# Kernel optimization log

Hardware: AMD Instinct MI355X
Metric: run time of the kernel (lower is better)

The kernel has to match this reference:

```python
import jax, jax.numpy as jnp
import numpy as np
import math

N_HEADS = 4
GROUPS = 32
EPS = 1e-5


def group_norm(x, w, b, groups=GROUPS):
    B, C, H, W = x.shape
    xg = x.reshape(B, groups, C // groups, H, W)
    mu = xg.mean(axis=(2, 3, 4), keepdims=True)
    var = xg.var(axis=(2, 3, 4), keepdims=True)
    xn = ((xg - mu) / jnp.sqrt(var + EPS)).reshape(B, C, H, W)
    return xn * w[None, :, None, None] + b[None, :, None, None]


def setup_inputs() -> dict:
    key = jax.random.key(0)
    ks = jax.random.split(key, 8)
    B, C, H, W = 4, 256, 64, 64
    s = 1.0 / math.sqrt(C)
    return {
        "x": jax.random.normal(ks[0], (B, C, H, W), jnp.float32),
        "context": jax.random.normal(ks[1], (B, C, H, W), jnp.float32),
        "gn_q_w": jnp.ones((C,), jnp.float32),
        "gn_q_b": jnp.zeros((C,), jnp.float32),
        "gn_ctx_w": jnp.ones((C,), jnp.float32),
        "gn_ctx_b": jnp.zeros((C,), jnp.float32),
        "Wq": jax.random.normal(ks[2], (C, C), jnp.float32) * s,
        "Wk": jax.random.normal(ks[3], (C, C), jnp.float32) * s,
        "Wv": jax.random.normal(ks[4], (C, C), jnp.float32) * s,
        "Wo": jax.random.normal(ks[5], (C, C), jnp.float32) * s,
        "bo": jnp.zeros((C,), jnp.float32),
    }


def reference(x, context, gn_q_w, gn_q_b, gn_ctx_w, gn_ctx_b, Wq, Wk, Wv, Wo, bo):
    B, C, H, W = x.shape
    hd = C // N_HEADS
    # 1x1 convs == channel matmuls
    q = jnp.einsum('oc,bchw->bohw', Wq, group_norm(x, gn_q_w, gn_q_b))
    k = jnp.einsum('oc,bchw->bohw', Wk, group_norm(context, gn_ctx_w, gn_ctx_b))
    v = jnp.einsum('oc,bchw->bohw', Wv, context)
    q = q.reshape(B, N_HEADS, hd, H * W)
    k = k.reshape(B, N_HEADS, hd, H * W)
    v = v.reshape(B, N_HEADS, hd, H * W)
    attn = jnp.einsum('bncd,bnce->bnde', q, k) / math.sqrt(hd)  # [B,n,HW,HW]
    attn = jax.nn.softmax(attn, axis=-1)
    out = jnp.einsum('bnde,bnce->bncd', attn, v).reshape(B, C, H, W)
    out = jnp.einsum('oc,bchw->bohw', Wo, out) + bo[None, :, None, None]
    return x + out
```

## Files before the change

kernel.cpp:

```cpp
#include <hip/hip_runtime.h>

typedef __bf16 bf16x8 __attribute__((ext_vector_type(8)));
typedef __bf16 bf16x2 __attribute__((ext_vector_type(2)));
typedef float f32x2 __attribute__((ext_vector_type(2)));
typedef float f32x4 __attribute__((ext_vector_type(4)));
typedef float f32x16 __attribute__((ext_vector_type(16)));

#define DEV static __device__ __forceinline__

DEV unsigned short f2bf(float f) {
  union { float f; unsigned int u; } v; v.f = f;
  unsigned int u = v.u;
  return (unsigned short)((u + 0x7FFFu + ((u >> 16) & 1u)) >> 16);
}

DEV bf16x8 ldb8(const unsigned short* p) { return *reinterpret_cast<const bf16x8*>(p); }

DEV bf16x8 ldsb8(const unsigned short* base, int byteoff) {
  return *reinterpret_cast<const bf16x8*>((const char*)base + byteoff);
}

DEV f32x4 mfma(bf16x8 a, bf16x8 b, f32x4 c) {
  return __builtin_amdgcn_mfma_f32_16x16x32_bf16(a, b, c, 0, 0, 0);
}
DEV f32x16 mfma32(bf16x8 a, bf16x8 b, f32x16 c) {
  return __builtin_amdgcn_mfma_f32_32x32x16_bf16(a, b, c, 0, 0, 0);
}

DEV float fexp2(float x) {
  float r;
  asm("v_exp_f32 %0, %1" : "=v"(r) : "v"(x));
  return r;
}

DEV unsigned cvtpk(float a, float b) {
  f32x2 t = {a, b};
  bf16x2 r = __builtin_convertvector(t, bf16x2);
  return __builtin_bit_cast(unsigned, r);
}

DEV bf16x8 pack4(unsigned w0, unsigned w1, unsigned w2, unsigned w3) {
  union { unsigned u[4]; bf16x8 v; } x;
  x.u[0] = w0; x.u[1] = w1; x.u[2] = w2; x.u[3] = w3;
  return x.v;
}

DEV f32x16 zero16() {
  f32x16 z;
#pragma unroll
  for (int i = 0; i < 16; ++i) z[i] = 0.f;
  return z;
}

__global__ __launch_bounds__(1024) void gn_stats_kernel(
    const float* __restrict__ x, const float* __restrict__ ctx,
    const float* __restrict__ gqw, const float* __restrict__ gqb,
    const float* __restrict__ gcw, const float* __restrict__ gcb,
    float* __restrict__ ssbuf) {
  int id = blockIdx.x;
  int tensor = id >> 7;
  int bg = id & 127;
  int b = bg >> 5, g = bg & 31;
  const float* src = tensor ? ctx : x;
  const float* gw = tensor ? gcw : gqw;
  const float* gb = tensor ? gcb : gqb;
  float* scale = ssbuf + tensor * 2048;
  float* shift = scale + 1024;

  const float* base = src + (size_t)(b * 256 + g * 8) * 4096;
  int tid = threadIdx.x;
  float s = 0.f, sq = 0.f;
#pragma unroll
  for (int i = 0; i < 8; ++i) {
    float4 v = *reinterpret_cast<const float4*>(base + (i * 1024 + tid) * 4);
    s += v.x + v.y + v.z + v.w;
    sq = __builtin_fmaf(v.x, v.x, sq);
    sq = __builtin_fmaf(v.y, v.y, sq);
    sq = __builtin_fmaf(v.z, v.z, sq);
    sq = __builtin_fmaf(v.w, v.w, sq);
  }
#pragma unroll
  for (int sh = 32; sh; sh >>= 1) {
    s += __shfl_down(s, sh);
    sq += __shfl_down(sq, sh);
  }
  __shared__ float rs[16], rq[16], mr[2];
  int w = tid >> 6;
  if ((tid & 63) == 0) { rs[w] = s; rq[w] = sq; }
  __syncthreads();
  if (tid == 0) {
    float S = 0.f, Q = 0.f;
#pragma unroll
    for (int i = 0; i < 16; ++i) { S += rs[i]; Q += rq[i]; }
    float mean = S * (1.f / 32768.f);
    float var = __builtin_fmaf(-mean, mean, Q * (1.f / 32768.f));
    mr[0] = mean;
    mr[1] = rsqrtf(var + 1e-5f);
  }
  __syncthreads();
  if (tid < 8) {
    int c = g * 8 + tid;
    float sc = gw[c] * mr[1];
    scale[b * 256 + c] = sc;
    shift[b * 256 + c] = __builtin_fmaf(-mr[0], sc, gb[c]);
  }
}

template <int OUTMODE>
__global__ __launch_bounds__(1024) void proj_kernel(
    const float* __restrict__ W, const float* __restrict__ in,
    const float* __restrict__ scale, const float* __restrict__ shift,
    unsigned short* __restrict__ out, float wscale) {
  __shared__ unsigned short Alds[128][72];
  __shared__ unsigned short Blds[128][72];
  const int b = blockIdx.z;
  const int o0 = blockIdx.y * 128;
  const int p0 = blockIdx.x * 128;
  const int tid = threadIdx.x;
  const int w = tid >> 6, lane = tid & 63;
  const int g = lane >> 4, l15 = lane & 15;
  const int oh = (w >> 2) * 32, ph = (w & 3) * 32;

  f32x4 acc[2][2];
#pragma unroll
  for (int i = 0; i < 2; ++i)
#pragma unroll
    for (int j = 0; j < 2; ++j) acc[i][j] = (f32x4){0.f, 0.f, 0.f, 0.f};

  for (int kk = 0; kk < 4; ++kk) {
    const int c0 = kk * 64;
    __syncthreads();
#pragma unroll
    for (int i = 0; i < 2; ++i) {
      int idx = i * 1024 + tid;
      int row = idx >> 4, col4 = (idx & 15) * 4;
      float4 wv = *reinterpret_cast<const float4*>(&W[(size_t)(o0 + row) * 256 + c0 + col4]);
      ushort4 bv = {f2bf(wv.x * wscale), f2bf(wv.y * wscale),
                    f2bf(wv.z * wscale), f2bf(wv.w * wscale)};
      *reinterpret_cast<ushort4*>(&Alds[row][col4]) = bv;
    }
#pragma unroll
    for (int i = 0; i < 2; ++i) {
      int idx = i * 1024 + tid;
      int cc = idx >> 5, p4 = (idx & 31) * 4;
      int c = c0 + cc;
      float4 xv = *reinterpret_cast<const float4*>(&in[((size_t)b * 256 + c) * 4096 + p0 + p4]);
      float sc = 1.f, sh = 0.f;
      if (scale) { sc = scale[b * 256 + c]; sh = shift[b * 256 + c]; }
      Blds[p4 + 0][cc] = f2bf(__builtin_fmaf(xv.x, sc, sh));
      Blds[p4 + 1][cc] = f2bf(__builtin_fmaf(xv.y, sc, sh));
      Blds[p4 + 2][cc] = f2bf(__builtin_fmaf(xv.z, sc, sh));
      Blds[p4 + 3][cc] = f2bf(__builtin_fmaf(xv.w, sc, sh));
    }
    __syncthreads();
#pragma unroll
    for (int kf = 0; kf < 2; ++kf) {
      bf16x8 av[2], bv[2];
#pragma unroll
      for (int mf = 0; mf < 2; ++mf) av[mf] = ldb8(&Alds[oh + mf * 16 + l15][kf * 32 + g * 8]);
#pragma unroll
      for (int nf = 0; nf < 2; ++nf) bv[nf] = ldb8(&Blds[ph + nf * 16 + l15][kf * 32 + g * 8]);
#pragma unroll
      for (int mf = 0; mf < 2; ++mf)
#pragma unroll
        for (int nf = 0; nf < 2; ++nf) acc[mf][nf] = mfma(av[mf], bv[nf], acc[mf][nf]);
    }
  }
#pragma unroll
  for (int mf = 0; mf < 2; ++mf)
#pragma unroll
    for (int nf = 0; nf < 2; ++nf) {
      int o = o0 + oh + mf * 16 + g * 4;
      int p = p0 + ph + nf * 16 + l15;
      if (OUTMODE == 0) {
        int h = o >> 6, ch = o & 63;
        ushort4 vv = {f2bf(acc[mf][nf][0]), f2bf(acc[mf][nf][1]),
                      f2bf(acc[mf][nf][2]), f2bf(acc[mf][nf][3])};
        *reinterpret_cast<ushort4*>(&out[(((size_t)b * 4 + h) * 4096 + p) * 64 + ch]) = vv;
      } else {
#pragma unroll
        for (int r = 0; r < 4; ++r) {
          int oo = o + r;
          out[(((size_t)b * 4 + (oo >> 6)) * 64 + (oo & 63)) * 4096 + p] = f2bf(acc[mf][nf][r]);
        }
      }
    }
}

DEV void stageK32(const unsigned short* kg, int e0, char* ldsbase, int tidg) {
  int o = tidg * 16;
  int r = o >> 7;
  int col = (o & 127) ^ ((r & 7) << 4);
  const char* src = (const char*)(kg + (size_t)(e0 + r) * 64) + col;
  __builtin_amdgcn_global_load_lds(
      (__attribute__((address_space(1))) void*)src,
      (__attribute__((address_space(3))) void*)(ldsbase + (tidg >> 6) * 1024), 16, 0, 0);
}

DEV void stageV32(const unsigned short* vg, int e0, char* ldsbase, int tidg) {
  int o = tidg * 16;
  int c = o >> 6;
  int slotL = ((o >> 4) & 3) ^ ((c >> 1) & 3);
  const char* src = (const char*)(vg + (size_t)c * 4096 + e0 + slotL * 8);
  __builtin_amdgcn_global_load_lds(
      (__attribute__((address_space(1))) void*)src,
      (__attribute__((address_space(3))) void*)(ldsbase + (tidg >> 6) * 1024), 16, 0, 0);
}

__global__ __launch_bounds__(1024) void attn_kernel(
    const unsigned short* __restrict__ QT, const unsigned short* __restrict__ KT,
    const unsigned short* __restrict__ V, unsigned short* __restrict__ OT) {
  __shared__ __align__(16) char smem[67584];
  const int bh = blockIdx.x;
  const int tid = threadIdx.x;
  const int w = tid >> 6, lane = tid & 63;
  const int g = w >> 2, wl = w & 3;
  const int tidg = tid & 255;
  const int hi = lane >> 5, l31 = lane & 31;
  const int d = blockIdx.y * 128 + wl * 32 + l31;

  char* Kb0 = smem + g * 16384;
  char* Kb1 = Kb0 + 4096;
  char* Vb0 = Kb0 + 8192;
  char* Vb1 = Kb0 + 12288;

  const unsigned short* kg = KT + (size_t)bh * 4096 * 64;
  const unsigned short* vg = V + (size_t)bh * 64 * 4096;

  bf16x8 q[4];
#pragma unroll
  for (int ks = 0; ks < 4; ++ks)
    q[ks] = ldb8(&QT[((size_t)bh * 4096 + d) * 64 + ks * 16 + hi * 8]);

  f32x16 oacc[2];
  oacc[0] = zero16();
  oacc[1] = zero16();
  float lsum = 0.f;
  const int kswz = (l31 & 7) << 4;
  const int vswz = ((l31 >> 1) & 3) << 4;
  const int E0 = g * 1024;

  auto compute = [&](const char* kb_, const char* vb_) {
    const unsigned short* kb = (const unsigned short*)kb_;
    const unsigned short* vb = (const unsigned short*)vb_;
    f32x16 st = zero16();
    __builtin_amdgcn_s_setprio(1);
#pragma unroll
    for (int ks = 0; ks < 4; ++ks) {
      bf16x8 k0 = ldsb8(kb, l31 * 128 + ((ks * 32 + hi * 16) ^ kswz));
      st = mfma32(k0, q[ks], st);
    }
    __builtin_amdgcn_s_setprio(0);

#pragma unroll
    for (int i = 0; i < 16; ++i) st[i] = fexp2(st[i]);

    bf16x8 pf[2];
#pragma unroll
    for (int sh = 0; sh < 2; ++sh) {
      const int rb = sh * 8;
      unsigned a0 = cvtpk(st[rb + 0], st[rb + 1]);
      unsigned b0 = cvtpk(st[rb + 4], st[rb + 5]);
      unsigned a1 = cvtpk(st[rb + 2], st[rb + 3]);
      unsigned b1 = cvtpk(st[rb + 6], st[rb + 7]);
      auto r0 = __builtin_amdgcn_permlane32_swap(a0, b0, false, false);
      auto r1 = __builtin_amdgcn_permlane32_swap(a1, b1, false, false);
      pf[sh] = pack4(r0[0], r1[0], r0[1], r1[1]);
    }

    float ss[8];
#pragma unroll
    for (int i = 0; i < 8; ++i) ss[i] = st[i] + st[i + 8];
#pragma unroll
    for (int s2 = 4; s2 > 0; s2 >>= 1)
#pragma unroll
      for (int i = 0; i < s2; ++i) ss[i] += ss[i + s2];
    lsum += ss[0] + __shfl_xor(ss[0], 32);

#pragma unroll
    for (int s = 0; s < 2; ++s) {
      bf16x8 v0 = ldsb8(vb, l31 * 64 + ((s * 32 + hi * 16) ^ vswz));
      bf16x8 v1 = ldsb8(vb, (32 + l31) * 64 + ((s * 32 + hi * 16) ^ vswz));
      __builtin_amdgcn_s_setprio(1);
      oacc[0] = mfma32(v0, pf[s], oacc[0]);
      oacc[1] = mfma32(v1, pf[s], oacc[1]);
      __builtin_amdgcn_s_setprio(0);
    }
  };

  stageK32(kg, E0, Kb0, tidg);
  stageV32(vg, E0, Vb0, tidg);
  __syncthreads();

  for (int t2 = 0; t2 < 16; ++t2) {
    const int e = E0 + t2 * 64;
    stageK32(kg, e + 32, Kb1, tidg);
    stageV32(vg, e + 32, Vb1, tidg);
    compute(Kb0, Vb0);
    __syncthreads();
    if (t2 < 15) {
      stageK32(kg, e + 64, Kb0, tidg);
      stageV32(vg, e + 64, Vb0, tidg);
    }
    compute(Kb1, Vb1);
    __syncthreads();
  }

  float* slab = (float*)smem;
  float* myA = slab + (wl * 64 + lane) * 33;
  float* myB = myA + 256 * 33;
  if (g == 1 || g == 3) {
    float* p = (g == 1) ? myA : myB;
#pragma unroll
    for (int i = 0; i < 16; ++i) { p[i] = oacc[0][i]; p[16 + i] = oacc[1][i]; }
    p[32] = lsum;
  }
  __syncthreads();
  if (g == 0) {
#pragma unroll
    for (int i = 0; i < 16; ++i) { oacc[0][i] += myA[i]; oacc[1][i] += myA[16 + i]; }
    lsum += myA[32];
  }
  if (g == 2) {
#pragma unroll
    for (int i = 0; i < 16; ++i) { oacc[0][i] += myB[i]; oacc[1][i] += myB[16 + i]; }
    lsum += myB[32];
  }
  __syncthreads();
  if (g == 2) {
#pragma unroll
    for (int i = 0; i < 16; ++i) { myA[i] = oacc[0][i]; myA[16 + i] = oacc[1][i]; }
    myA[32] = lsum;
  }
  __syncthreads();
  if (g == 0) {
#pragma unroll
    for (int i = 0; i < 16; ++i) { oacc[0][i] += myA[i]; oacc[1][i] += myA[16 + i]; }
    lsum += myA[32];
    float inv = 1.f / lsum;
    size_t obase = ((size_t)bh * 4096 + d) * 64;
#pragma unroll
    for (int cb = 0; cb < 2; ++cb)
#pragma unroll
      for (int gq = 0; gq < 4; ++gq) {
        ushort4 sv;
        sv.x = f2bf(oacc[cb][gq * 4 + 0] * inv);
        sv.y = f2bf(oacc[cb][gq * 4 + 1] * inv);
        sv.z = f2bf(oacc[cb][gq * 4 + 2] * inv);
        sv.w = f2bf(oacc[cb][gq * 4 + 3] * inv);
        *reinterpret_cast<ushort4*>(&OT[obase + cb * 32 + gq * 8 + hi * 4]) = sv;
      }
  }
}

__global__ __launch_bounds__(1024) void final_kernel(
    const float* __restrict__ Wo, const unsigned short* __restrict__ OT,
    const float* __restrict__ bo, const float* __restrict__ x,
    float* __restrict__ out) {
  __shared__ unsigned short Alds[128][72];
  __shared__ unsigned short Blds[128][72];
  const int b = blockIdx.z;
  const int o0 = blockIdx.y * 128;
  const int p0 = blockIdx.x * 128;
  const int tid = threadIdx.x;
  const int w = tid >> 6, lane = tid & 63;
  const int g = lane >> 4, l15 = lane & 15;
  const int oh = (w >> 2) * 32, ph = (w & 3) * 32;

  f32x4 acc[2][2];
#pragma unroll
  for (int i = 0; i < 2; ++i)
#pragma unroll
    for (int j = 0; j < 2; ++j) acc[i][j] = (f32x4){0.f, 0.f, 0.f, 0.f};

  for (int kk = 0; kk < 4; ++kk) {
    const int c0 = kk * 64;
    __syncthreads();
#pragma unroll
    for (int i = 0; i < 2; ++i) {
      int idx = i * 1024 + tid;
      int row = idx >> 4, col4 = (idx & 15) * 4;
      float4 wv = *reinterpret_cast<const float4*>(&Wo[(size_t)(o0 + row) * 256 + c0 + col4]);
      ushort4 bv = {f2bf(wv.x), f2bf(wv.y), f2bf(wv.z), f2bf(wv.w)};
      *reinterpret_cast<ushort4*>(&Alds[row][col4]) = bv;
    }
    {
      int idx = tid;
      int row = idx >> 3, c8 = (idx & 7) * 8;
      *reinterpret_cast<uint4*>(&Blds[row][c8]) =
          *reinterpret_cast<const uint4*>(&OT[(((size_t)b * 4 + kk) * 4096 + p0 + row) * 64 + c8]);
    }
    __syncthreads();
#pragma unroll
    for (int kf = 0; kf < 2; ++kf) {
      bf16x8 av[2], bv[2];
#pragma unroll
      for (int mf = 0; mf < 2; ++mf) av[mf] = ldb8(&Alds[oh + mf * 16 + l15][kf * 32 + g * 8]);
#pragma unroll
      for (int nf = 0; nf < 2; ++nf) bv[nf] = ldb8(&Blds[ph + nf * 16 + l15][kf * 32 + g * 8]);
#pragma unroll
      for (int mf = 0; mf < 2; ++mf)
#pragma unroll
        for (int nf = 0; nf < 2; ++nf) acc[mf][nf] = mfma(av[mf], bv[nf], acc[mf][nf]);
    }
  }
#pragma unroll
  for (int mf = 0; mf < 2; ++mf)
#pragma unroll
    for (int nf = 0; nf < 2; ++nf) {
      int o = o0 + oh + mf * 16 + g * 4;
      int p = p0 + ph + nf * 16 + l15;
#pragma unroll
      for (int r = 0; r < 4; ++r) {
        size_t idx = ((size_t)b * 256 + o + r) * 4096 + p;
        out[idx] = acc[mf][nf][r] + bo[o + r] + x[idx];
      }
    }
}

extern "C" void kernel_launch(void* const* d_in, const int* in_sizes, int n_in,
                              void* d_out, int out_size, void* d_ws, size_t ws_size,
                              hipStream_t stream) {
  const float* x = (const float*)d_in[0];
  const float* ctx = (const float*)d_in[1];
  const float* gqw = (const float*)d_in[2];
  const float* gqb = (const float*)d_in[3];
  const float* gcw = (const float*)d_in[4];
  const float* gcb = (const float*)d_in[5];
  const float* Wq = (const float*)d_in[6];
  const float* Wk = (const float*)d_in[7];
  const float* Wv = (const float*)d_in[8];
  const float* Wo = (const float*)d_in[9];
  const float* bo = (const float*)d_in[10];
  float* out = (float*)d_out;

  char* ws = (char*)d_ws;
  float* ssbuf = (float*)ws;
  float* scaleQ = ssbuf;
  float* shiftQ = ssbuf + 1024;
  float* scaleK = ssbuf + 2048;
  float* shiftK = ssbuf + 3072;
  const size_t TEN = (size_t)4 * 4 * 4096 * 64;
  unsigned short* QT = (unsigned short*)(ws + 65536);
  unsigned short* KT = QT + TEN;
  unsigned short* Vb = KT + TEN;
  unsigned short* OT = Vb + TEN;

  gn_stats_kernel<<<256, 1024, 0, stream>>>(x, ctx, gqw, gqb, gcw, gcb, ssbuf);

  const float beta = 0.125f * 1.44269504088896340736f;
  dim3 pg(32, 2, 4);
  proj_kernel<0><<<pg, 1024, 0, stream>>>(Wq, x, scaleQ, shiftQ, QT, beta);
  proj_kernel<0><<<pg, 1024, 0, stream>>>(Wk, ctx, scaleK, shiftK, KT, 1.f);
  proj_kernel<1><<<pg, 1024, 0, stream>>>(Wv, ctx, nullptr, nullptr, Vb, 1.f);

  attn_kernel<<<dim3(16, 32), 1024, 0, stream>>>(QT, KT, Vb, OT);

  final_kernel<<<dim3(32, 2, 4), 1024, 0, stream>>>(Wo, OT, bo, x, out);
}
```

Baseline: 148.7 us.

## Triple-buffer attention K/V staging and merge QKV projections into one launch

The attention kernel moves from double-buffered K/V LDS staging with two full __syncthreads per pair of tiles to a three-slot ring. Each step waits with s_waitcnt vmcnt(2) plus a barrier, so two tiles of loads stay in flight while one is computed. LDS use rises from about 66KB to 96KB per block. Separately, the three Q/K/V projection launches become a single launch that selects weights, input and output layout by blockIdx.y, which removes two kernel launches and lets all projection blocks run together.

```diff
diff --git a/kernel.cpp b/kernel.cpp
--- a/kernel.cpp
+++ b/kernel.cpp
@@ -106,16 +106,26 @@
   }
 }
 
-template <int OUTMODE>
-__global__ __launch_bounds__(1024) void proj_kernel(
-    const float* __restrict__ W, const float* __restrict__ in,
-    const float* __restrict__ scale, const float* __restrict__ shift,
-    unsigned short* __restrict__ out, float wscale) {
+__global__ __launch_bounds__(1024) void qkv_kernel(
+    const float* __restrict__ x, const float* __restrict__ ctx,
+    const float* __restrict__ ssbuf,
+    const float* __restrict__ Wq, const float* __restrict__ Wk,
+    const float* __restrict__ Wv,
+    unsigned short* __restrict__ QT, unsigned short* __restrict__ KT,
+    unsigned short* __restrict__ Vb, float beta) {
   __shared__ unsigned short Alds[128][72];
   __shared__ unsigned short Blds[128][72];
+  const int which = blockIdx.y >> 1;
+  const int o0 = (blockIdx.y & 1) * 128;
   const int b = blockIdx.z;
-  const int o0 = blockIdx.y * 128;
   const int p0 = blockIdx.x * 128;
+  const float* W = which == 0 ? Wq : (which == 1 ? Wk : Wv);
+  const float* in = which == 0 ? x : ctx;
+  const float* scale = which == 0 ? ssbuf : (which == 1 ? ssbuf + 2048 : nullptr);
+  const float* shift = which == 0 ? ssbuf + 1024 : (which == 1 ? ssbuf + 3072 : nullptr);
+  unsigned short* out = which == 0 ? QT : (which == 1 ? KT : Vb);
+  const float wscale = which == 0 ? beta : 1.f;
+
   const int tid = threadIdx.x;
   const int w = tid >> 6, lane = tid & 63;
   const int g = lane >> 4, l15 = lane & 15;
@@ -172,7 +182,7 @@
     for (int nf = 0; nf < 2; ++nf) {
       int o = o0 + oh + mf * 16 + g * 4;
       int p = p0 + ph + nf * 16 + l15;
-      if (OUTMODE == 0) {
+      if (which < 2) {
         int h = o >> 6, ch = o & 63;
         ushort4 vv = {f2bf(acc[mf][nf][0]), f2bf(acc[mf][nf][1]),
                       f2bf(acc[mf][nf][2]), f2bf(acc[mf][nf][3])};
@@ -210,7 +220,7 @@
 __global__ __launch_bounds__(1024) void attn_kernel(
     const unsigned short* __restrict__ QT, const unsigned short* __restrict__ KT,
     const unsigned short* __restrict__ V, unsigned short* __restrict__ OT) {
-  __shared__ __align__(16) char smem[67584];
+  __shared__ __align__(16) char smem[98304];
   const int bh = blockIdx.x;
   const int tid = threadIdx.x;
   const int w = tid >> 6, lane = tid & 63;
@@ -219,10 +229,7 @@
   const int hi = lane >> 5, l31 = lane & 31;
   const int d = blockIdx.y * 128 + wl * 32 + l31;
 
-  char* Kb0 = smem + g * 16384;
-  char* Kb1 = Kb0 + 4096;
-  char* Vb0 = Kb0 + 8192;
-  char* Vb1 = Kb0 + 12288;
+  char* gbase = smem + g * 24576;
 
   const unsigned short* kg = KT + (size_t)bh * 4096 * 64;
   const unsigned short* vg = V + (size_t)bh * 64 * 4096;
@@ -240,9 +247,15 @@
   const int vswz = ((l31 >> 1) & 3) << 4;
   const int E0 = g * 1024;
 
-  auto compute = [&](const char* kb_, const char* vb_) {
-    const unsigned short* kb = (const unsigned short*)kb_;
-    const unsigned short* vb = (const unsigned short*)vb_;
+  auto stage = [&](int t, int bi) {
+    char* kb = gbase + bi * 8192;
+    stageK32(kg, E0 + t * 32, kb, tidg);
+    stageV32(vg, E0 + t * 32, kb + 4096, tidg);
+  };
+
+  auto compute = [&](int bi) {
+    const unsigned short* kb = (const unsigned short*)(gbase + bi * 8192);
+    const unsigned short* vb = (const unsigned short*)(gbase + bi * 8192 + 4096);
     f32x16 st = zero16();
     __builtin_amdgcn_s_setprio(1);
 #pragma unroll
@@ -288,23 +301,18 @@
     }
   };
 
-  stageK32(kg, E0, Kb0, tidg);
-  stageV32(vg, E0, Vb0, tidg);
-  __syncthreads();
-
-  for (int t2 = 0; t2 < 16; ++t2) {
-    const int e = E0 + t2 * 64;
-    stageK32(kg, e + 32, Kb1, tidg);
-    stageV32(vg, e + 32, Vb1, tidg);
-    compute(Kb0, Vb0);
-    __syncthreads();
-    if (t2 < 15) {
-      stageK32(kg, e + 64, Kb0, tidg);
-      stageV32(vg, e + 64, Vb0, tidg);
-    }
-    compute(Kb1, Vb1);
-    __syncthreads();
-  }
+  stage(0, 0);
+  stage(1, 1);
+
+  for (int i = 0; i < 32; ++i) {
+    if (i < 31)
+      asm volatile("s_waitcnt vmcnt(2)\n\ts_barrier" ::: "memory");
+    else
+      asm volatile("s_waitcnt vmcnt(0)\n\ts_barrier" ::: "memory");
+    if (i + 2 < 32) stage(i + 2, (i + 2) % 3);
+    compute(i % 3);
+  }
+  __syncthreads();
 
   float* slab = (float*)smem;
   float* myA = slab + (wl * 64 + lane) * 33;
@@ -436,10 +444,6 @@
 
   char* ws = (char*)d_ws;
   float* ssbuf = (float*)ws;
-  float* scaleQ = ssbuf;
-  float* shiftQ = ssbuf + 1024;
-  float* scaleK = ssbuf + 2048;
-  float* shiftK = ssbuf + 3072;
   const size_t TEN = (size_t)4 * 4 * 4096 * 64;
   unsigned short* QT = (unsigned short*)(ws + 65536);
   unsigned short* KT = QT + TEN;
@@ -449,10 +453,8 @@
   gn_stats_kernel<<<256, 1024, 0, stream>>>(x, ctx, gqw, gqb, gcw, gcb, ssbuf);
 
   const float beta = 0.125f * 1.44269504088896340736f;
-  dim3 pg(32, 2, 4);
-  proj_kernel<0><<<pg, 1024, 0, stream>>>(Wq, x, scaleQ, shiftQ, QT, beta);
-  proj_kernel<0><<<pg, 1024, 0, stream>>>(Wk, ctx, scaleK, shiftK, KT, 1.f);
-  proj_kernel<1><<<pg, 1024, 0, stream>>>(Wv, ctx, nullptr, nullptr, Vb, 1.f);
+  qkv_kernel<<<dim3(32, 6, 4), 1024, 0, stream>>>(x, ctx, ssbuf, Wq, Wk, Wv,
+                                                  QT, KT, Vb, beta);
 
   attn_kernel<<<dim3(16, 32), 1024, 0, stream>>>(QT, KT, Vb, OT);
 
```

New measurement: 147.4 us. Within noise of the previous version (-0.9%).
